# Optimization experiments

Hardware: AMD Instinct MI355X
Metric: run time of the kernel (lower is better)

The kernel has to match this reference:

```python
import jax, jax.numpy as jnp
import numpy as np

R_EARTH = 6371.0


def haversine(coords):
    # coords: (B, N, 2) lat/lon in degrees -> (B, N, N) distances in km
    lat = jnp.deg2rad(coords[..., 0])
    lon = jnp.deg2rad(coords[..., 1])
    lat1, lon1 = lat[:, :, None], lon[:, :, None]   # (B,N,1)
    lat2, lon2 = lat[:, None, :], lon[:, None, :]   # (B,1,N)
    dlat, dlon = lat2 - lat1, lon2 - lon1
    a = jnp.sin(dlat / 2) ** 2 + jnp.cos(lat1) * jnp.cos(lat2) * jnp.sin(dlon / 2) ** 2
    a = jnp.clip(a, 0.0, 1.0)
    c = 2.0 * jnp.arctan2(jnp.sqrt(a), jnp.sqrt(1.0 - a))
    return R_EARTH * c


def setup_inputs() -> dict:
    key = jax.random.key(0)
    ks = jax.random.split(key, 16)
    B, N, T, D, H = 4, 256, 128, 512, 8
    hd = D // H
    s = 1.0 / np.sqrt(D)
    inp = {
        'x': jax.random.normal(ks[0], (B, N, T, D), dtype=jnp.float32),
        'coords': jax.random.uniform(ks[1], (B, N, 2), dtype=jnp.float32) * 90.0,
        'station_mask': jax.random.randint(ks[2], (B, N), 0, 2, dtype=jnp.int32),
        'Wq': jax.random.normal(ks[3], (D, D), dtype=jnp.float32) * s,
        'bq': jnp.zeros((D,), dtype=jnp.float32),
        'Wk': jax.random.normal(ks[4], (D, D), dtype=jnp.float32) * s,
        'bk': jnp.zeros((D,), dtype=jnp.float32),
        'Wv': jax.random.normal(ks[5], (D, D), dtype=jnp.float32) * s,
        'bv': jnp.zeros((D,), dtype=jnp.float32),
        'Wo': jax.random.normal(ks[6], (D, D), dtype=jnp.float32) * s,
        'bo': jnp.zeros((D,), dtype=jnp.float32),
        'Wd1': jax.random.normal(ks[7], (hd, 1), dtype=jnp.float32),
        'bd1': jnp.zeros((hd,), dtype=jnp.float32),
        'Wd2': jax.random.normal(ks[8], (H, hd), dtype=jnp.float32) / np.sqrt(hd),
        'bd2': jnp.zeros((H,), dtype=jnp.float32),
    }
    return inp


def reference(x, coords, station_mask, Wq, bq, Wk, bk, Wv, bv, Wo, bo, Wd1, bd1, Wd2, bd2):
    B, N, T, D = x.shape
    H = Wd2.shape[0]
    hd = D // H
    scale = jnp.sqrt(jnp.asarray(hd, dtype=x.dtype))

    x_repr = x.mean(axis=2)  # (B,N,D) temporal pooling

    def proj(W, b):
        y = x_repr @ W.T + b                       # (B,N,D)
        return y.reshape(B, N, H, hd).transpose(0, 2, 1, 3)  # (B,H,N,hd)

    Q, K, V = proj(Wq, bq), proj(Wk, bk), proj(Wv, bv)
    scores = jnp.einsum('bhnd,bhmd->bhnm', Q, K) / scale  # (B,H,N,N)

    # haversine distance -> 2-layer MLP bias, (B,N,N,H) -> (B,H,N,N)
    dist = haversine(coords)[..., None]                    # (B,N,N,1)
    hmid = jax.nn.relu(dist @ Wd1.T + bd1)                 # (B,N,N,hd)
    bias = (hmid @ Wd2.T + bd2).transpose(0, 3, 1, 2)      # (B,H,N,N)
    scores = scores + bias

    # mask invalid key stations
    scores = jnp.where(station_mask[:, None, None, :] == 0, -jnp.inf, scores)
    w = jax.nn.softmax(scores, axis=-1)

    out = jnp.einsum('bhnm,bhmd->bhnd', w, V)
    out = out.transpose(0, 2, 1, 3).reshape(B, N, D)
    out = out @ Wo.T + bo
    return jnp.broadcast_to(out[:, :, None, :], (B, N, T, D))
```

## Files before the change

### kernel.cpp

```cpp
#include <hip/hip_runtime.h>
#include <math.h>

#define Bc 4
#define Nc 256
#define Tc 128
#define Dc 512
#define Hc 8
#define HDc 64

typedef float f4v __attribute__((ext_vector_type(4)));

#define SWZ(row, k4) (((row) << 4) | ((k4) ^ (((row) >> 2) & 15)))

__global__ __launch_bounds__(256) void mean_kernel(const float* __restrict__ x,
                                                   float* __restrict__ xr) {
    const int bn = blockIdx.x;
    const int col = threadIdx.x & 127;
    const int half = threadIdx.x >> 7;
    const f4v* xp = (const f4v*)x + (size_t)bn * (Tc * Dc / 4)
                    + (size_t)(half * 64) * (Dc / 4) + col;
    f4v a[8];
#pragma unroll
    for (int u = 0; u < 8; ++u) a[u] = (f4v)(0.f);
    for (int t = 0; t < 64; t += 8) {
#pragma unroll
        for (int u = 0; u < 8; ++u)
            a[u] += __builtin_nontemporal_load(xp + (size_t)(t + u) * (Dc / 4));
    }
    f4v s = ((a[0] + a[1]) + (a[2] + a[3])) + ((a[4] + a[5]) + (a[6] + a[7]));
    __shared__ f4v red[256];
    red[threadIdx.x] = s;
    __syncthreads();
    if (threadIdx.x < 128) {
        f4v r = (red[threadIdx.x] + red[threadIdx.x + 128]) * (1.0f / Tc);
        ((f4v*)xr)[(size_t)bn * (Dc / 4) + threadIdx.x] = r;
    }
}

__device__ __forceinline__ void gemm_core(const float* __restrict__ A,
                                          const float* __restrict__ W,
                                          int i0, int j0, float acc[4][4]) {
    __shared__ float4 As4[1024];
    __shared__ float4 Ws4[1024];
    const int tid = threadIdx.x;
    const int ty = tid >> 4, tx = tid & 15;
    float4 pa[4], pw[4];
#pragma unroll
    for (int p = 0; p < 4; ++p) {
        pa[p] = *(const float4*)&A[(size_t)(i0 + p * 16 + ty) * Dc + tx * 4];
        pw[p] = *(const float4*)&W[(size_t)(j0 + p * 16 + ty) * Dc + tx * 4];
    }
    for (int kb = 0; kb < 8; ++kb) {
#pragma unroll
        for (int p = 0; p < 4; ++p) {
            As4[SWZ(p * 16 + ty, tx)] = pa[p];
            Ws4[SWZ(p * 16 + ty, tx)] = pw[p];
        }
        __syncthreads();
        if (kb < 7) {
            const int k0 = (kb + 1) * 64;
#pragma unroll
            for (int p = 0; p < 4; ++p) {
                pa[p] = *(const float4*)&A[(size_t)(i0 + p * 16 + ty) * Dc + k0 + tx * 4];
                pw[p] = *(const float4*)&W[(size_t)(j0 + p * 16 + ty) * Dc + k0 + tx * 4];
            }
        }
#pragma unroll
        for (int kk4 = 0; kk4 < 16; ++kk4) {
            float4 a[4], w[4];
#pragma unroll
            for (int q = 0; q < 4; ++q) a[q] = As4[SWZ(ty * 4 + q, kk4)];
#pragma unroll
            for (int c = 0; c < 4; ++c) w[c] = Ws4[SWZ(tx * 4 + c, kk4)];
#pragma unroll
            for (int q = 0; q < 4; ++q)
#pragma unroll
                for (int c = 0; c < 4; ++c) {
                    acc[q][c] += a[q].x * w[c].x;
                    acc[q][c] += a[q].y * w[c].y;
                    acc[q][c] += a[q].z * w[c].z;
                    acc[q][c] += a[q].w * w[c].w;
                }
        }
        __syncthreads();
    }
}

__global__ __launch_bounds__(256) void qkv_kernel(
    const float* __restrict__ xr, const float* __restrict__ Wq, const float* __restrict__ bq,
    const float* __restrict__ Wk, const float* __restrict__ bk,
    const float* __restrict__ Wv, const float* __restrict__ bv,
    float* __restrict__ Yq, float* __restrict__ Kt, float* __restrict__ Yv) {
    const int it = blockIdx.x;
    const int mat = blockIdx.y >> 3;
    const int jt = blockIdx.y & 7;
    const float* W = (mat == 0) ? Wq : (mat == 1) ? Wk : Wv;
    const float* bias = (mat == 0) ? bq : (mat == 1) ? bk : bv;
    const int i0 = it * 64, j0 = jt * 64;
    float acc[4][4] = {{0.f}};
    gemm_core(xr, W, i0, j0, acc);
    const int ty = threadIdx.x >> 4, tx = threadIdx.x & 15;
    if (mat == 1) {
        const int b = i0 >> 8;
        const int n0 = (i0 & 255) + ty * 4;
#pragma unroll
        for (int c = 0; c < 4; ++c) {
            const int j = j0 + tx * 4 + c;
            const float bj = bias[j];
            float4 v = make_float4(acc[0][c] + bj, acc[1][c] + bj,
                                   acc[2][c] + bj, acc[3][c] + bj);
            *(float4*)&Kt[(((size_t)b * Hc + jt) * HDc + (tx * 4 + c)) * Nc + n0] = v;
        }
    } else {
        float* Y = (mat == 0) ? Yq : Yv;
#pragma unroll
        for (int r = 0; r < 4; ++r) {
            const int i = i0 + ty * 4 + r;
            const int j = j0 + tx * 4;
            float4 o = make_float4(acc[r][0] + bias[j + 0], acc[r][1] + bias[j + 1],
                                   acc[r][2] + bias[j + 2], acc[r][3] + bias[j + 3]);
            *(float4*)&Y[(size_t)i * Dc + j] = o;
        }
    }
}

__global__ __launch_bounds__(256) void attn_kernel(
    const float* __restrict__ Yq, const float* __restrict__ Kt,
    const float* __restrict__ Yv, const float* __restrict__ coords,
    const int* __restrict__ mask, const float* __restrict__ Wd1,
    const float* __restrict__ bd1, const float* __restrict__ Wd2,
    const float* __restrict__ bd2, float* __restrict__ attnO) {
    const int bh = blockIdx.x >> 6;
    const int ng = blockIdx.x & 63;
    const int b = bh >> 3, h = bh & 7;
    const int tid = threadIdx.x;
    const int wave = tid >> 6, lane = tid & 63;
    const int n = ng * 4 + wave;

    __shared__ float sq[4][64];
    __shared__ float sw[4][256];
    __shared__ float slat[256], slon[256], scl[256];
    __shared__ float swd1[64], sbd1[64], swd2[64];
    __shared__ int smk[256];

    {
        const float DEG = 0.017453292519943295f;
        float la = coords[((size_t)b * Nc + tid) * 2 + 0] * DEG;
        float lo = coords[((size_t)b * Nc + tid) * 2 + 1] * DEG;
        slat[tid] = la; slon[tid] = lo; scl[tid] = cosf(la);
        smk[tid] = mask[(size_t)b * Nc + tid];
        if (tid < 64) {
            swd1[tid] = Wd1[tid];
            sbd1[tid] = bd1[tid];
            swd2[tid] = Wd2[h * 64 + tid];
        }
    }
    sq[wave][lane] = Yq[((size_t)(b * Nc + n)) * Dc + h * HDc + lane] * 0.125f;
    __syncthreads();

    const float4* ktp = (const float4*)(Kt + (size_t)bh * HDc * Nc);
    float4 acc = make_float4(0.f, 0.f, 0.f, 0.f);
#pragma unroll 16
    for (int k = 0; k < 64; ++k) {
        const float qk = sq[wave][k];
        const float4 kv = ktp[k * 64 + lane];
        acc.x += qk * kv.x; acc.y += qk * kv.y;
        acc.z += qk * kv.z; acc.w += qk * kv.w;
    }

    const float lat1 = slat[n], lon1 = slon[n], cl1 = scl[n];
    float dist[4];
#pragma unroll
    for (int j = 0; j < 4; ++j) {
        const int m = lane * 4 + j;
        float sdlat = sinf((slat[m] - lat1) * 0.5f);
        float sdlon = sinf((slon[m] - lon1) * 0.5f);
        float a = sdlat * sdlat + cl1 * scl[m] * sdlon * sdlon;
        a = fminf(fmaxf(a, 0.f), 1.f);
        dist[j] = 12742.0f * atan2f(sqrtf(a), sqrtf(1.0f - a));
    }
    const float b2 = bd2[h];
    float bias[4] = {b2, b2, b2, b2};
#pragma unroll 4
    for (int k = 0; k < 64; ++k) {
        const float w1 = swd1[k], c1 = sbd1[k], w2 = swd2[k];
#pragma unroll
        for (int j = 0; j < 4; ++j)
            bias[j] += fmaxf(dist[j] * w1 + c1, 0.f) * w2;
    }
    float s[4] = {acc.x + bias[0], acc.y + bias[1], acc.z + bias[2], acc.w + bias[3]};
#pragma unroll
    for (int j = 0; j < 4; ++j)
        if (smk[lane * 4 + j] == 0) s[j] = -1e30f;

    float mx = fmaxf(fmaxf(s[0], s[1]), fmaxf(s[2], s[3]));
#pragma unroll
    for (int off = 32; off > 0; off >>= 1) mx = fmaxf(mx, __shfl_xor(mx, off, 64));
    float e0 = expf(s[0] - mx), e1 = expf(s[1] - mx);
    float e2 = expf(s[2] - mx), e3 = expf(s[3] - mx);
    ((float4*)sw[wave])[lane] = make_float4(e0, e1, e2, e3);
    float sum = e0 + e1 + e2 + e3;
#pragma unroll
    for (int off = 32; off > 0; off >>= 1) sum += __shfl_xor(sum, off, 64);
    const float inv = 1.0f / sum;
    __syncthreads();

    const int mo = lane >> 4, d4 = lane & 15;
    const float* vbase = Yv + (size_t)b * Nc * Dc + h * HDc + d4 * 4;
    const float* wv = sw[wave];
    float4 o = make_float4(0.f, 0.f, 0.f, 0.f);
#pragma unroll 8
    for (int mq = 0; mq < 64; ++mq) {
        const int m = mq * 4 + mo;
        const float wm = wv[m];
        const float4 v = *(const float4*)&vbase[(size_t)m * Dc];
        o.x += wm * v.x; o.y += wm * v.y; o.z += wm * v.z; o.w += wm * v.w;
    }
#pragma unroll
    for (int off = 16; off <= 32; off <<= 1) {
        o.x += __shfl_xor(o.x, off, 64);
        o.y += __shfl_xor(o.y, off, 64);
        o.z += __shfl_xor(o.z, off, 64);
        o.w += __shfl_xor(o.w, off, 64);
    }
    if (mo == 0) {
        float4 r = make_float4(o.x * inv, o.y * inv, o.z * inv, o.w * inv);
        *(float4*)&attnO[((size_t)(b * Nc + n)) * Dc + h * HDc + d4 * 4] = r;
    }
}

__global__ __launch_bounds__(256) void oproj_bcast_kernel(
    const float* __restrict__ attnI, const float* __restrict__ Wo,
    const float* __restrict__ bo, float* __restrict__ out) {
    const int i0 = blockIdx.x * 64, j0 = blockIdx.y * 64;
    const int z = blockIdx.z;
    float acc[4][4] = {{0.f}};
    gemm_core(attnI, Wo, i0, j0, acc);

    __shared__ f4v tile[1024];
    const int ty = threadIdx.x >> 4, tx = threadIdx.x & 15;
#pragma unroll
    for (int q = 0; q < 4; ++q) {
        const int j = j0 + tx * 4;
        f4v v;
        v.x = acc[q][0] + bo[j + 0]; v.y = acc[q][1] + bo[j + 1];
        v.z = acc[q][2] + bo[j + 2]; v.w = acc[q][3] + bo[j + 3];
        tile[(ty * 4 + q) * 16 + tx] = v;
    }
    __syncthreads();

    const int d4 = threadIdx.x & 15;
    const int sub = threadIdx.x >> 4;
    for (int r = 0; r < 64; ++r) {
        const f4v val = tile[r * 16 + d4];
        float* rowbase = out + (size_t)(i0 + r) * Tc * Dc + j0;
#pragma unroll
        for (int tt = 0; tt < 4; ++tt) {
            const int t = z * 64 + tt * 16 + sub;
            __builtin_nontemporal_store(val, (f4v*)(rowbase + (size_t)t * Dc) + d4);
        }
    }
}

extern "C" void kernel_launch(void* const* d_in, const int* in_sizes, int n_in,
                              void* d_out, int out_size, void* d_ws, size_t ws_size,
                              hipStream_t stream) {
    const float* x      = (const float*)d_in[0];
    const float* coords = (const float*)d_in[1];
    const int*   smask  = (const int*)d_in[2];
    const float* Wq = (const float*)d_in[3];  const float* bq = (const float*)d_in[4];
    const float* Wk = (const float*)d_in[5];  const float* bk = (const float*)d_in[6];
    const float* Wv = (const float*)d_in[7];  const float* bv = (const float*)d_in[8];
    const float* Wo = (const float*)d_in[9];  const float* bo = (const float*)d_in[10];
    const float* Wd1 = (const float*)d_in[11]; const float* bd1 = (const float*)d_in[12];
    const float* Wd2 = (const float*)d_in[13]; const float* bd2 = (const float*)d_in[14];
    float* out = (float*)d_out;

    float* ws    = (float*)d_ws;
    const size_t BND = (size_t)Bc * Nc * Dc;
    float* xr    = ws;
    float* Yq    = xr + BND;
    float* Kt    = Yq + BND;
    float* Yv    = Kt + BND;
    float* attn  = Yv + BND;

    mean_kernel<<<Bc * Nc, 256, 0, stream>>>(x, xr);
    qkv_kernel<<<dim3(16, 24), 256, 0, stream>>>(xr, Wq, bq, Wk, bk, Wv, bv, Yq, Kt, Yv);
    attn_kernel<<<Bc * Hc * (Nc / 4), 256, 0, stream>>>(Yq, Kt, Yv, coords, smask,
                                                        Wd1, bd1, Wd2, bd2, attn);
    oproj_bcast_kernel<<<dim3(16, 8, 2), 256, 0, stream>>>(attn, Wo, bo, out);
}
```

Measured before the change: 594.5 us.

## Process four queries per wave in attention kernel to reuse K/V loads

```diff
diff --git a/kernel.cpp b/kernel.cpp
--- a/kernel.cpp
+++ b/kernel.cpp
@@ -130,15 +130,16 @@
     const int* __restrict__ mask, const float* __restrict__ Wd1,
     const float* __restrict__ bd1, const float* __restrict__ Wd2,
     const float* __restrict__ bd2, float* __restrict__ attnO) {
-    const int bh = blockIdx.x >> 6;
-    const int ng = blockIdx.x & 63;
+    const int bh = blockIdx.x >> 4;
+    const int g = blockIdx.x & 15;
     const int b = bh >> 3, h = bh & 7;
     const int tid = threadIdx.x;
-    const int wave = tid >> 6, lane = tid & 63;
-    const int n = ng * 4 + wave;
-
-    __shared__ float sq[4][64];
-    __shared__ float sw[4][256];
+    const int wid = tid >> 6, lane = tid & 63;
+    const int n_base = g * 16;
+    const int q0 = wid * 4;
+
+    __shared__ float sq[16][64];
+    __shared__ float sw[16][256];
     __shared__ float slat[256], slon[256], scl[256];
     __shared__ float swd1[64], sbd1[64], swd2[64];
     __shared__ int smk[256];
@@ -147,85 +148,101 @@
         const float DEG = 0.017453292519943295f;
         float la = coords[((size_t)b * Nc + tid) * 2 + 0] * DEG;
         float lo = coords[((size_t)b * Nc + tid) * 2 + 1] * DEG;
-        slat[tid] = la; slon[tid] = lo; scl[tid] = cosf(la);
+        slat[tid] = la; slon[tid] = lo; scl[tid] = __cosf(la);
         smk[tid] = mask[(size_t)b * Nc + tid];
         if (tid < 64) {
             swd1[tid] = Wd1[tid];
             sbd1[tid] = bd1[tid];
             swd2[tid] = Wd2[h * 64 + tid];
         }
-    }
-    sq[wave][lane] = Yq[((size_t)(b * Nc + n)) * Dc + h * HDc + lane] * 0.125f;
+#pragma unroll
+        for (int r = 0; r < 4; ++r) {
+            const int idx = r * 256 + tid;
+            const int nl = idx >> 6, d = idx & 63;
+            sq[nl][d] = Yq[((size_t)(b * Nc + n_base + nl)) * Dc + h * HDc + d] * 0.125f;
+        }
+    }
     __syncthreads();
 
     const float4* ktp = (const float4*)(Kt + (size_t)bh * HDc * Nc);
-    float4 acc = make_float4(0.f, 0.f, 0.f, 0.f);
-#pragma unroll 16
+    f4v acc[4];
+#pragma unroll
+    for (int j = 0; j < 4; ++j) acc[j] = (f4v)(0.f);
+#pragma unroll 8
     for (int k = 0; k < 64; ++k) {
-        const float qk = sq[wave][k];
         const float4 kv = ktp[k * 64 + lane];
-        acc.x += qk * kv.x; acc.y += qk * kv.y;
-        acc.z += qk * kv.z; acc.w += qk * kv.w;
-    }
-
-    const float lat1 = slat[n], lon1 = slon[n], cl1 = scl[n];
-    float dist[4];
+        const f4v kvv = {kv.x, kv.y, kv.z, kv.w};
+#pragma unroll
+        for (int j = 0; j < 4; ++j) acc[j] += sq[q0 + j][k] * kvv;
+    }
+
+    float inv[4];
+    const int mbase = lane * 4;
+    float mlat[4], mlon[4], mcl[4];
+    int mk[4];
+#pragma unroll
+    for (int jm = 0; jm < 4; ++jm) {
+        mlat[jm] = slat[mbase + jm]; mlon[jm] = slon[mbase + jm];
+        mcl[jm] = scl[mbase + jm];   mk[jm] = smk[mbase + jm];
+    }
 #pragma unroll
     for (int j = 0; j < 4; ++j) {
-        const int m = lane * 4 + j;
-        float sdlat = sinf((slat[m] - lat1) * 0.5f);
-        float sdlon = sinf((slon[m] - lon1) * 0.5f);
-        float a = sdlat * sdlat + cl1 * scl[m] * sdlon * sdlon;
-        a = fminf(fmaxf(a, 0.f), 1.f);
-        dist[j] = 12742.0f * atan2f(sqrtf(a), sqrtf(1.0f - a));
-    }
-    const float b2 = bd2[h];
-    float bias[4] = {b2, b2, b2, b2};
-#pragma unroll 4
-    for (int k = 0; k < 64; ++k) {
-        const float w1 = swd1[k], c1 = sbd1[k], w2 = swd2[k];
-#pragma unroll
-        for (int j = 0; j < 4; ++j)
-            bias[j] += fmaxf(dist[j] * w1 + c1, 0.f) * w2;
-    }
-    float s[4] = {acc.x + bias[0], acc.y + bias[1], acc.z + bias[2], acc.w + bias[3]};
-#pragma unroll
-    for (int j = 0; j < 4; ++j)
-        if (smk[lane * 4 + j] == 0) s[j] = -1e30f;
-
-    float mx = fmaxf(fmaxf(s[0], s[1]), fmaxf(s[2], s[3]));
-#pragma unroll
-    for (int off = 32; off > 0; off >>= 1) mx = fmaxf(mx, __shfl_xor(mx, off, 64));
-    float e0 = expf(s[0] - mx), e1 = expf(s[1] - mx);
-    float e2 = expf(s[2] - mx), e3 = expf(s[3] - mx);
-    ((float4*)sw[wave])[lane] = make_float4(e0, e1, e2, e3);
-    float sum = e0 + e1 + e2 + e3;
-#pragma unroll
-    for (int off = 32; off > 0; off >>= 1) sum += __shfl_xor(sum, off, 64);
-    const float inv = 1.0f / sum;
+        const int n = n_base + q0 + j;
+        const float lat1 = slat[n], lon1 = slon[n], cl1 = scl[n];
+        float s[4];
+#pragma unroll
+        for (int jm = 0; jm < 4; ++jm) {
+            float sdlat = __sinf((mlat[jm] - lat1) * 0.5f);
+            float sdlon = __sinf((mlon[jm] - lon1) * 0.5f);
+            float a = sdlat * sdlat + cl1 * mcl[jm] * sdlon * sdlon;
+            a = fminf(fmaxf(a, 0.f), 1.f);
+            float dist = 12742.0f * atan2f(sqrtf(a), sqrtf(1.0f - a));
+            float bias = 0.f;
+#pragma unroll 8
+            for (int k = 0; k < 64; ++k)
+                bias += fmaxf(dist * swd1[k] + sbd1[k], 0.f) * swd2[k];
+            s[jm] = acc[j][jm] + bias + bd2[h];
+            if (mk[jm] == 0) s[jm] = -1e30f;
+        }
+        float mx = fmaxf(fmaxf(s[0], s[1]), fmaxf(s[2], s[3]));
+#pragma unroll
+        for (int off = 32; off > 0; off >>= 1) mx = fmaxf(mx, __shfl_xor(mx, off, 64));
+        float e0 = __expf(s[0] - mx), e1 = __expf(s[1] - mx);
+        float e2 = __expf(s[2] - mx), e3 = __expf(s[3] - mx);
+        ((float4*)sw[q0 + j])[lane] = make_float4(e0, e1, e2, e3);
+        float sum = e0 + e1 + e2 + e3;
+#pragma unroll
+        for (int off = 32; off > 0; off >>= 1) sum += __shfl_xor(sum, off, 64);
+        inv[j] = 1.0f / sum;
+    }
     __syncthreads();
 
     const int mo = lane >> 4, d4 = lane & 15;
     const float* vbase = Yv + (size_t)b * Nc * Dc + h * HDc + d4 * 4;
-    const float* wv = sw[wave];
-    float4 o = make_float4(0.f, 0.f, 0.f, 0.f);
+    f4v o[4];
+#pragma unroll
+    for (int j = 0; j < 4; ++j) o[j] = (f4v)(0.f);
 #pragma unroll 8
     for (int mq = 0; mq < 64; ++mq) {
         const int m = mq * 4 + mo;
-        const float wm = wv[m];
-        const float4 v = *(const float4*)&vbase[(size_t)m * Dc];
-        o.x += wm * v.x; o.y += wm * v.y; o.z += wm * v.z; o.w += wm * v.w;
-    }
-#pragma unroll
-    for (int off = 16; off <= 32; off <<= 1) {
-        o.x += __shfl_xor(o.x, off, 64);
-        o.y += __shfl_xor(o.y, off, 64);
-        o.z += __shfl_xor(o.z, off, 64);
-        o.w += __shfl_xor(o.w, off, 64);
-    }
-    if (mo == 0) {
-        float4 r = make_float4(o.x * inv, o.y * inv, o.z * inv, o.w * inv);
-        *(float4*)&attnO[((size_t)(b * Nc + n)) * Dc + h * HDc + d4 * 4] = r;
+        const f4v v = *(const f4v*)&vbase[(size_t)m * Dc];
+#pragma unroll
+        for (int j = 0; j < 4; ++j) o[j] += sw[q0 + j][m] * v;
+    }
+#pragma unroll
+    for (int j = 0; j < 4; ++j) {
+#pragma unroll
+        for (int off = 16; off <= 32; off <<= 1) {
+            o[j].x += __shfl_xor(o[j].x, off, 64);
+            o[j].y += __shfl_xor(o[j].y, off, 64);
+            o[j].z += __shfl_xor(o[j].z, off, 64);
+            o[j].w += __shfl_xor(o[j].w, off, 64);
+        }
+        if (mo == 0) {
+            const int n = n_base + q0 + j;
+            f4v r = o[j] * inv[j];
+            *(f4v*)&attnO[((size_t)(b * Nc + n)) * Dc + h * HDc + d4 * 4] = r;
+        }
     }
 }
 
@@ -286,7 +303,7 @@
 
     mean_kernel<<<Bc * Nc, 256, 0, stream>>>(x, xr);
     qkv_kernel<<<dim3(16, 24), 256, 0, stream>>>(xr, Wq, bq, Wk, bk, Wv, bv, Yq, Kt, Yv);
-    attn_kernel<<<Bc * Hc * (Nc / 4), 256, 0, stream>>>(Yq, Kt, Yv, coords, smask,
-                                                        Wd1, bd1, Wd2, bd2, attn);
+    attn_kernel<<<32 * 16, 256, 0, stream>>>(Yq, Kt, Yv, coords, smask,
+                                             Wd1, bd1, Wd2, bd2, attn);
     oproj_bcast_kernel<<<dim3(16, 8, 2), 256, 0, stream>>>(attn, Wo, bo, out);
 }
```

New measurement: 587.4 us. About the same (-1.2%).
